# Kernel tuning notes

Hardware: AMD Instinct MI355X
Metric: run time of the kernel (lower is better)

The kernel has to match this reference:

```python
import jax, jax.numpy as jnp
import numpy as np
import math

B, S, K, H, NH = 4, 1024, 512, 1024, 16
HD = H // NH  # 64


def _split_heads(x):
    # [B, L, H] -> [B, NH, L, HD]
    b, l, _ = x.shape
    return x.reshape(b, l, NH, HD).transpose(0, 2, 1, 3)


def setup_inputs() -> dict:
    key = jax.random.key(0)
    ks = jax.random.split(key, 16)
    scale = 1.0 / math.sqrt(H)
    d = {
        'hidden_states': jax.random.normal(ks[0], (B, S, H), jnp.float32),
        'encoder_hidden_states': jax.random.normal(ks[1], (B, K, H), jnp.float32),
        'attention_mask': jnp.zeros((B, 1, 1, S), jnp.float32),
        'encoder_attention_mask': jnp.zeros((B, 1, 1, K), jnp.float32),
    }
    names = ['q', 'k', 'v', 'kq', 'kk', 'kv']
    for i, n in enumerate(names):
        d[f'W{n}'] = jax.random.normal(ks[2 + i], (H, H), jnp.float32) * scale
        d[f'b{n}'] = jnp.zeros((H,), jnp.float32)
    return d


def reference(hidden_states, encoder_hidden_states, attention_mask, encoder_attention_mask,
              Wq, bq, Wk, bk, Wv, bv, Wkq, bkq, Wkk, bkk, Wkv, bkv):
    inv = 1.0 / math.sqrt(HD)
    # self branch
    q = _split_heads(hidden_states @ Wq + bq)            # [B,NH,S,HD]
    k = _split_heads(hidden_states @ Wk + bk)
    v = _split_heads(hidden_states @ Wv + bv)
    scores = jnp.einsum('bhsd,bhtd->bhst', q, k) * inv + attention_mask
    probs = jax.nn.softmax(scores, axis=-1)              # [B,NH,S,S]
    ctx = jnp.einsum('bhst,bhtd->bhsd', probs, v)
    # knowledge branch
    kq = _split_heads(hidden_states @ Wkq + bkq)          # [B,NH,S,HD]
    kk = _split_heads(encoder_hidden_states @ Wkk + bkk)  # [B,NH,K,HD]
    kv = _split_heads(encoder_hidden_states @ Wkv + bkv)
    kscores = jnp.einsum('bhsd,bhtd->bhst', kq, kk) * inv + encoder_attention_mask
    kprobs = jax.nn.softmax(kscores, axis=-1)            # [B,NH,S,K]
    kctx = jnp.einsum('bhst,bhtd->bhsd', kprobs, kv)
    # merge heads and average branches
    out = (ctx + kctx) * 0.5                             # [B,NH,S,HD]
    out = out.transpose(0, 2, 1, 3).reshape(B, S, H)
    return out
```

## Files before the change

### kernel.cpp

```cpp
#include <hip/hip_runtime.h>

#define BATCH 4
#define SEQ   1024
#define KENC  512
#define HDIM  1024
#define NHEAD 16
#define HD    64
#define LOG2E 1.44269504088896340736f

typedef __attribute__((ext_vector_type(8))) short bf16x8;
typedef __attribute__((ext_vector_type(4))) float f32x4;
typedef __attribute__((ext_vector_type(4))) float f4v;
typedef __attribute__((ext_vector_type(4))) short s4v;

__device__ __forceinline__ short f2bf(float f) {
  unsigned u = __float_as_uint(f);
  u += 0x7fffu + ((u >> 16) & 1u);
  return (short)(u >> 16);
}

__device__ __forceinline__ void gload_lds16(const void* g, void* l) {
  __builtin_amdgcn_global_load_lds(
      (const __attribute__((address_space(1))) void*)g,
      (__attribute__((address_space(3))) void*)l, 16, 0, 0);
}

template <int C>
__device__ __forceinline__ float dppf(float x) {
  return __int_as_float(
      __builtin_amdgcn_update_dpp(0, __float_as_int(x), C, 0xF, 0xF, false));
}
__device__ __forceinline__ float red16_max(float x) {
  x = fmaxf(x, dppf<0xB1>(x));
  x = fmaxf(x, dppf<0x4E>(x));
  x = fmaxf(x, dppf<0x141>(x));
  x = fmaxf(x, dppf<0x140>(x));
  return x;
}
__device__ __forceinline__ float red16_sum(float x) {
  x += dppf<0xB1>(x);
  x += dppf<0x4E>(x);
  x += dppf<0x141>(x);
  x += dppf<0x140>(x);
  return x;
}

__global__ __launch_bounds__(256) void cast_bf16(const float* __restrict__ src,
                                                 short* __restrict__ dst, int n4) {
  int i = blockIdx.x * 256 + threadIdx.x;
  if (i >= n4) return;
  f4v v = ((const f4v*)src)[i];
  s4v o;
#pragma unroll
  for (int j = 0; j < 4; ++j) o[j] = f2bf(v[j]);
  ((s4v*)dst)[i] = o;
}

struct WtArgs { const float* W[6]; };

__global__ __launch_bounds__(256) void wt_cast(WtArgs a, short* __restrict__ wt) {
  int j = blockIdx.z;
  const float* W = a.W[j];
  short* dst = wt + (size_t)j * (HDIM * HDIM);
  int cb = blockIdx.x * 32, rb = blockIdx.y * 32;
  __shared__ float t[32][33];
  int tx = threadIdx.x & 31, ty = threadIdx.x >> 5;
#pragma unroll
  for (int rr = 0; rr < 4; ++rr)
    t[ty + rr * 8][tx] = W[(size_t)(rb + ty + rr * 8) * HDIM + cb + tx];
  __syncthreads();
#pragma unroll
  for (int rr = 0; rr < 4; ++rr)
    dst[(size_t)(cb + ty + rr * 8) * HDIM + rb + tx] = f2bf(t[tx][ty + rr * 8]);
}

struct ProjArgs {
  const short* X[6];
  const short* Wt[6];
  const float* bias[6];
  short* out[6];
  int M[6];
  int tshift[6];
  int mode[6];
  float scale[6];
};

__global__ __launch_bounds__(256) void proj_gemm(ProjArgs a) {
  int job = blockIdx.z;
  int M = a.M[job];
  int by = blockIdx.y;
  if (by * 128 >= M) return;
  int bx = blockIdx.x;
  const short* X = a.X[job];
  const short* W = a.Wt[job];

  __shared__ short As[128 * 32];
  __shared__ short Bs[128 * 32];

  int tid = threadIdx.x, lane = tid & 63, wave = tid >> 6;
  int wr = wave >> 1, wc = wave & 1;
  int l15 = lane & 15, g4 = lane >> 4;

  f32x4 acc[4][4];
#pragma unroll
  for (int m = 0; m < 4; ++m)
#pragma unroll
    for (int n = 0; n < 4; ++n)
#pragma unroll
      for (int r = 0; r < 4; ++r) acc[m][n][r] = 0.0f;

  int arow = by * 128, brow = bx * 128;
  const int crow = lane >> 2;
  const int sgrp = (lane & 3) ^ ((lane >> 2) & 3) ^ (lane >> 4);
  const int rsw = (lane & 3) ^ ((l15) >> 2);

  for (int k0 = 0; k0 < HDIM; k0 += 32) {
#pragma unroll
    for (int cc = 0; cc < 2; ++cc) {
      int c = wave * 2 + cc;
      gload_lds16(X + (size_t)(arow + c * 16 + crow) * HDIM + k0 + sgrp * 8,
                  (char*)As + c * 1024);
      gload_lds16(W + (size_t)(brow + c * 16 + crow) * HDIM + k0 + sgrp * 8,
                  (char*)Bs + c * 1024);
    }
    __syncthreads();
    bf16x8 af[4], bfr[4];
#pragma unroll
    for (int m = 0; m < 4; ++m)
      af[m] = *(const bf16x8*)((const char*)As + (wr * 64 + m * 16 + l15) * 64 +
                               ((g4 ^ rsw) << 4));
#pragma unroll
    for (int n = 0; n < 4; ++n)
      bfr[n] = *(const bf16x8*)((const char*)Bs + (wc * 64 + n * 16 + l15) * 64 +
                                ((g4 ^ rsw) << 4));
#pragma unroll
    for (int m = 0; m < 4; ++m)
#pragma unroll
      for (int n = 0; n < 4; ++n)
        acc[m][n] = __builtin_amdgcn_mfma_f32_16x16x32_bf16(af[m], bfr[n],
                                                            acc[m][n], 0, 0, 0);
    __syncthreads();
  }

  const float* bias = a.bias[job];
  short* out = a.out[job];
  int tshift = a.tshift[job], tmask = (1 << tshift) - 1, mode = a.mode[job];
  float scl = a.scale[job];
#pragma unroll
  for (int m = 0; m < 4; ++m) {
    int rowb = arow + wr * 64 + m * 16 + (g4 << 2);
#pragma unroll
    for (int n = 0; n < 4; ++n) {
      int col = brow + wc * 64 + n * 16 + l15;
      float bv = bias[col];
      int head = col >> 6, d = col & 63;
#pragma unroll
      for (int r = 0; r < 4; ++r) {
        int row = rowb + r;
        int bb = row >> tshift, t = row & tmask;
        float val = (acc[m][n][r] + bv) * scl;
        size_t idx;
        if (mode == 0)
          idx = ((((size_t)bb * NHEAD + head) << tshift) + t) * 64 + d;
        else
          idx = ((((size_t)bb * NHEAD + head) * 64 + d) << tshift) + t;
        out[idx] = f2bf(val);
      }
    }
  }
}

__global__ __launch_bounds__(256, 3) void attn_kernel(
    const short* __restrict__ qall, const short* __restrict__ kall,
    const short* __restrict__ vTall, const short* __restrict__ kqall,
    const short* __restrict__ kkall, const short* __restrict__ kvTall,
    const float* __restrict__ amask, const float* __restrict__ emask,
    float* __restrict__ out) {
  __shared__ short Ks[2 * 64 * 64];
  __shared__ short Vs[2 * 64 * 64];
  __shared__ short Ps[4 * 16 * 64];

  int lid = blockIdx.x;
  int id = ((lid & 7) << 7) | (lid >> 3);
  int bh = id >> 4, qb = id & 15;
  int b = bh >> 4, h = bh & 15;
  int lane = threadIdx.x & 63, wave = threadIdx.x >> 6;
  int l15 = lane & 15, g4 = lane >> 4, l7 = lane & 7;
  int srow = lane >> 3;
  int scol = (l7 ^ srow) * 8;
  int qbase = qb * 64;
  char* Pw = (char*)(Ps + wave * 1024);

  const short* qp  = qall  + ((size_t)bh * SEQ + qbase + wave * 16) * 64;
  const short* kqp = kqall + ((size_t)bh * SEQ + qbase + wave * 16) * 64;
  bf16x8 qf0  = *(const bf16x8*)(qp  + l15 * 64 + g4 * 8);
  bf16x8 qf1  = *(const bf16x8*)(qp  + l15 * 64 + 32 + g4 * 8);
  bf16x8 kqf0 = *(const bf16x8*)(kqp + l15 * 64 + g4 * 8);
  bf16x8 kqf1 = *(const bf16x8*)(kqp + l15 * 64 + 32 + g4 * 8);

  const short* kp0 = kall   + (size_t)bh * SEQ * 64;
  const short* vp0 = vTall  + (size_t)bh * 64 * SEQ;
  const short* kp1 = kkall  + (size_t)bh * KENC * 64;
  const short* vp1 = kvTall + (size_t)bh * 64 * KENC;

  bf16x8 qc0 = qf0, qc1 = qf1;
  const float* mpc = amask + (size_t)b * SEQ;

  auto STAGE = [&](int pb, const short* kptr, const short* vptr, int Tt, int kt) {
#pragma unroll
    for (int cc = 0; cc < 2; ++cc) {
      int c = wave * 2 + cc;
      int row = c * 8 + srow;
      gload_lds16(kptr + (size_t)(kt * 64 + row) * 64 + scol,
                  (char*)Ks + pb * 8192 + c * 1024);
      gload_lds16(vptr + (size_t)row * Tt + kt * 64 + scol,
                  (char*)Vs + pb * 8192 + c * 1024);
    }
  };

  STAGE(0, kp0, vp0, SEQ, 0);

  f32x4 ctx[4], c1[4], mr, lr;
#pragma unroll
  for (int i = 0; i < 4; ++i) {
#pragma unroll
    for (int r = 0; r < 4; ++r) { ctx[i][r] = 0.0f; c1[i][r] = 0.0f; }
    mr[i] = -1e30f;
    lr[i] = 0.0f;
  }

#pragma unroll 2
  for (int t = 0; t < 24; ++t) {
    int p = t & 1;
    __syncthreads();
    if (t < 23) {
      int tn = t + 1;
      bool nb = tn >= 16;
      const short* skp = nb ? kp1 : kp0;
      const short* svp = nb ? vp1 : vp0;
      int sT = nb ? KENC : SEQ;
      int skt = nb ? tn - 16 : tn;
      STAGE(p ^ 1, skp, svp, sT, skt);
    }
    if (t == 16) {
#pragma unroll
      for (int dt = 0; dt < 4; ++dt) {
#pragma unroll
        for (int r = 0; r < 4; ++r) {
          c1[dt][r] = ctx[dt][r] * __builtin_amdgcn_rcpf(lr[r]);
          ctx[dt][r] = 0.0f;
        }
      }
#pragma unroll
      for (int r = 0; r < 4; ++r) { mr[r] = -1e30f; lr[r] = 0.0f; }
      qc0 = kqf0;
      qc1 = kqf1;
      mpc = emask + (size_t)b * KENC;
    }
    int kt = (t >= 16) ? t - 16 : t;
    const char* Kb = (const char*)Ks + p * 8192;
    const char* Vb = (const char*)Vs + p * 8192;

    float mk[4];
#pragma unroll
    for (int t2 = 0; t2 < 4; ++t2) mk[t2] = mpc[kt * 64 + t2 * 16 + l15] * LOG2E;

    f32x4 sc[4];
#pragma unroll
    for (int t2 = 0; t2 < 4; ++t2)
#pragma unroll
      for (int r = 0; r < 4; ++r) sc[t2][r] = 0.0f;

    __builtin_amdgcn_s_setprio(1);
#pragma unroll
    for (int t2 = 0; t2 < 4; ++t2) {
      bf16x8 kf0 = *(const bf16x8*)(Kb + (t2 * 16 + l15) * 128 + ((g4 ^ l7) << 4));
      bf16x8 kf1 = *(const bf16x8*)(Kb + (t2 * 16 + l15) * 128 + (((4 + g4) ^ l7) << 4));
      sc[t2] = __builtin_amdgcn_mfma_f32_16x16x32_bf16(qc0, kf0, sc[t2], 0, 0, 0);
      sc[t2] = __builtin_amdgcn_mfma_f32_16x16x32_bf16(qc1, kf1, sc[t2], 0, 0, 0);
    }
    __builtin_amdgcn_s_setprio(0);

#pragma unroll
    for (int t2 = 0; t2 < 4; ++t2)
#pragma unroll
      for (int r = 0; r < 4; ++r) sc[t2][r] += mk[t2];

    f32x4 rm;
#pragma unroll
    for (int r = 0; r < 4; ++r)
      rm[r] = fmaxf(fmaxf(sc[0][r], sc[1][r]), fmaxf(sc[2][r], sc[3][r]));
#pragma unroll
    for (int r = 0; r < 4; ++r) rm[r] = red16_max(rm[r]);

    int need = (rm[0] > mr[0] + 12.f) || (rm[1] > mr[1] + 12.f) ||
               (rm[2] > mr[2] + 12.f) || (rm[3] > mr[3] + 12.f);
    if (__any(need)) {
#pragma unroll
      for (int r = 0; r < 4; ++r) {
        float mn = fmaxf(mr[r], rm[r]);
        float s = __builtin_amdgcn_exp2f(mr[r] - mn);
        mr[r] = mn;
        lr[r] *= s;
        ctx[0][r] *= s; ctx[1][r] *= s; ctx[2][r] *= s; ctx[3][r] *= s;
      }
    }

    f32x4 pv[4], rs;
#pragma unroll
    for (int r = 0; r < 4; ++r) rs[r] = 0.0f;
#pragma unroll
    for (int t2 = 0; t2 < 4; ++t2)
#pragma unroll
      for (int r = 0; r < 4; ++r) {
        pv[t2][r] = __builtin_amdgcn_exp2f(sc[t2][r] - mr[r]);
        rs[r] += pv[t2][r];
      }
#pragma unroll
    for (int r = 0; r < 4; ++r) lr[r] += red16_sum(rs[r]);

#pragma unroll
    for (int t2 = 0; t2 < 4; ++t2) {
      int gg = t2 * 2 + (l15 >> 3);
#pragma unroll
      for (int r4 = 0; r4 < 4; ++r4) {
        int rr = g4 * 4 + r4;
        *(short*)(Pw + rr * 128 + (((gg ^ (rr & 7)) << 4) | (l7 * 2))) =
            f2bf(pv[t2][r4]);
      }
    }
    __builtin_amdgcn_s_setprio(1);
#pragma unroll
    for (int kc = 0; kc < 2; ++kc) {
      bf16x8 pf = *(const bf16x8*)(Pw + l15 * 128 + (((kc * 4 + g4) ^ l7) << 4));
#pragma unroll
      for (int dt = 0; dt < 4; ++dt) {
        bf16x8 vf = *(const bf16x8*)(Vb + (dt * 16 + l15) * 128 +
                                     (((kc * 4 + g4) ^ l7) << 4));
        ctx[dt] = __builtin_amdgcn_mfma_f32_16x16x32_bf16(pf, vf, ctx[dt], 0, 0, 0);
      }
    }
    __builtin_amdgcn_s_setprio(0);
  }

#pragma unroll
  for (int dt = 0; dt < 4; ++dt)
#pragma unroll
    for (int r = 0; r < 4; ++r) {
      float v2 = ctx[dt][r] * __builtin_amdgcn_rcpf(lr[r]);
      int s = qbase + wave * 16 + g4 * 4 + r;
      int d = dt * 16 + l15;
      out[((size_t)b * SEQ + s) * HDIM + h * 64 + d] = 0.5f * (c1[dt][r] + v2);
    }
}

extern "C" void kernel_launch(void* const* d_in, const int* in_sizes, int n_in,
                              void* d_out, int out_size, void* d_ws, size_t ws_size,
                              hipStream_t stream) {
  const float* hid = (const float*)d_in[0];
  const float* enc = (const float*)d_in[1];
  const float* amask = (const float*)d_in[2];
  const float* emask = (const float*)d_in[3];

  char* ws = (char*)d_ws;
  short* hbf = (short*)(ws);
  short* ebf = (short*)(ws + (8u << 20));
  short* wt = (short*)(ws + (12u << 20));
  short* qo = (short*)(ws + (24u << 20));
  short* ko = (short*)(ws + (32u << 20));
  short* vT = (short*)(ws + (40u << 20));
  short* kqo = (short*)(ws + (48u << 20));
  short* kko = (short*)(ws + (56u << 20));
  short* kvT = (short*)(ws + (60u << 20));

  cast_bf16<<<4096, 256, 0, stream>>>(hid, hbf, (BATCH * SEQ * HDIM) / 4);
  cast_bf16<<<2048, 256, 0, stream>>>(enc, ebf, (BATCH * KENC * HDIM) / 4);

  WtArgs wa;
  for (int j = 0; j < 6; ++j) wa.W[j] = (const float*)d_in[4 + 2 * j];
  wt_cast<<<dim3(32, 32, 6), 256, 0, stream>>>(wa, wt);

  ProjArgs pa;
  const short* Xs[6] = {hbf, hbf, hbf, hbf, ebf, ebf};
  short* outs[6] = {qo, ko, vT, kqo, kko, kvT};
  const int Ms[6] = {4096, 4096, 4096, 4096, 2048, 2048};
  const int tsh[6] = {10, 10, 10, 10, 9, 9};
  const int md[6] = {0, 0, 1, 0, 0, 1};
  const float qscale = 0.125f * LOG2E;
  const float scl[6] = {qscale, 1.f, 1.f, qscale, 1.f, 1.f};
  for (int j = 0; j < 6; ++j) {
    pa.X[j] = Xs[j];
    pa.Wt[j] = wt + (size_t)j * (HDIM * HDIM);
    pa.bias[j] = (const float*)d_in[5 + 2 * j];
    pa.out[j] = outs[j];
    pa.M[j] = Ms[j];
    pa.tshift[j] = tsh[j];
    pa.mode[j] = md[j];
    pa.scale[j] = scl[j];
  }
  proj_gemm<<<dim3(8, 32, 6), 256, 0, stream>>>(pa);

  attn_kernel<<<1024, 256, 0, stream>>>(qo, ko, vT, kqo, kko, kvT, amask, emask,
                                        (float*)d_out);
}
```

Baseline: 151.6 us.

## Fuse projection GEMMs into two wide 256x256 tiles with 4-stage LDS pipeline

Replaces the six-job 128x128 projection GEMM with two fused GEMMs: hidden states times four concatenated weights (N=4096) and encoder states times two (N=2048). It uses 256x256 tiles with 8 waves, a 4-deep LDS ring fed by async global-to-LDS loads over 64-element K steps, and split phases that interleave loads with MFMA under priority boosts. The intent is more operand reuse per byte loaded, overlap of loads with compute, and fewer blocks. In exchange it needs 128KB of LDS and many more accumulator registers, which limits occupancy, and 320 blocks may fill the CUs unevenly.

```diff
diff --git a/kernel.cpp b/kernel.cpp
--- a/kernel.cpp
+++ b/kernel.cpp
@@ -74,100 +74,170 @@
     dst[(size_t)(cb + ty + rr * 8) * HDIM + rb + tx] = f2bf(t[tx][ty + rr * 8]);
 }
 
-struct ProjArgs {
-  const short* X[6];
-  const short* Wt[6];
+struct GemmArgs {
+  const short* X[2];
+  const short* W[2];
   const float* bias[6];
   short* out[6];
-  int M[6];
-  int tshift[6];
-  int mode[6];
   float scale[6];
 };
 
-__global__ __launch_bounds__(256) void proj_gemm(ProjArgs a) {
-  int job = blockIdx.z;
-  int M = a.M[job];
-  int by = blockIdx.y;
-  if (by * 128 >= M) return;
-  int bx = blockIdx.x;
-  const short* X = a.X[job];
-  const short* W = a.Wt[job];
-
-  __shared__ short As[128 * 32];
-  __shared__ short Bs[128 * 32];
-
-  int tid = threadIdx.x, lane = tid & 63, wave = tid >> 6;
-  int wr = wave >> 1, wc = wave & 1;
+__global__ __launch_bounds__(512, 2) void proj_gemm8(GemmArgs a) {
+  __shared__ __align__(16) char Lds[131072];
+
+  int lid = blockIdx.x;
+  int id = (lid & 7) * 40 + (lid >> 3);
+  int job, bm, bn;
+  if (id < 256) { job = 0; bm = id >> 4; bn = id & 15; }
+  else          { job = 1; int i2 = id - 256; bm = i2 >> 3; bn = i2 & 7; }
+
+  const char* Xp = (const char*)a.X[job];
+  const char* Wp = (const char*)a.W[job];
+
+  int tid = threadIdx.x;
+  int lane = tid & 63, w = tid >> 6;
   int l15 = lane & 15, g4 = lane >> 4;
-
-  f32x4 acc[4][4];
-#pragma unroll
-  for (int m = 0; m < 4; ++m)
+  int wr = w >> 2, wc = w & 3;
+
+  int srow = w * 16 + (lane >> 2);
+  int sslot = (lane & 3) ^ ((lane >> 3) & 3);
+  size_t sa0 = ((size_t)(bm * 256 + srow)) * 2048 + sslot * 16;
+  size_t sa1 = ((size_t)(bm * 256 + 128 + srow)) * 2048 + sslot * 16;
+  size_t sb0 = ((size_t)(bn * 256 + srow)) * 2048 + sslot * 16;
+  size_t sb1 = ((size_t)(bn * 256 + 128 + srow)) * 2048 + sslot * 16;
+  int ldA0 = w * 1024, ldA1 = 8192 + w * 1024;
+  int ldB0 = 16384 + w * 1024, ldB1 = 24576 + w * 1024;
+
+  int slotR = (l15 >> 1) & 3;
+  int aoff = wr * 8192 + l15 * 64 + ((g4 ^ slotR) << 4);
+  int boff = 16384 + (wc >> 1) * 8192 + ((wc & 1) * 64 + l15) * 64 +
+             ((g4 ^ slotR) << 4);
+
+  f32x4 acc[8][4];
+#pragma unroll
+  for (int m = 0; m < 8; ++m)
 #pragma unroll
     for (int n = 0; n < 4; ++n)
 #pragma unroll
       for (int r = 0; r < 4; ++r) acc[m][n][r] = 0.0f;
 
-  int arow = by * 128, brow = bx * 128;
-  const int crow = lane >> 2;
-  const int sgrp = (lane & 3) ^ ((lane >> 2) & 3) ^ (lane >> 4);
-  const int rsw = (lane & 3) ^ ((l15) >> 2);
-
-  for (int k0 = 0; k0 < HDIM; k0 += 32) {
-#pragma unroll
-    for (int cc = 0; cc < 2; ++cc) {
-      int c = wave * 2 + cc;
-      gload_lds16(X + (size_t)(arow + c * 16 + crow) * HDIM + k0 + sgrp * 8,
-                  (char*)As + c * 1024);
-      gload_lds16(W + (size_t)(brow + c * 16 + crow) * HDIM + k0 + sgrp * 8,
-                  (char*)Bs + c * 1024);
-    }
-    __syncthreads();
-    bf16x8 af[4], bfr[4];
-#pragma unroll
-    for (int m = 0; m < 4; ++m)
-      af[m] = *(const bf16x8*)((const char*)As + (wr * 64 + m * 16 + l15) * 64 +
-                               ((g4 ^ rsw) << 4));
-#pragma unroll
-    for (int n = 0; n < 4; ++n)
-      bfr[n] = *(const bf16x8*)((const char*)Bs + (wc * 64 + n * 16 + l15) * 64 +
-                                ((g4 ^ rsw) << 4));
-#pragma unroll
-    for (int m = 0; m < 4; ++m)
-#pragma unroll
-      for (int n = 0; n < 4; ++n)
-        acc[m][n] = __builtin_amdgcn_mfma_f32_16x16x32_bf16(af[m], bfr[n],
-                                                            acc[m][n], 0, 0, 0);
-    __syncthreads();
+#define STG_A(bufo, kof)                                      \
+  do {                                                        \
+    gload_lds16(Xp + sa0 + (kof), Lds + (bufo) + ldA0);       \
+    gload_lds16(Xp + sa1 + (kof), Lds + (bufo) + ldA1);       \
+  } while (0)
+#define STG_B(bufo, kof)                                      \
+  do {                                                        \
+    gload_lds16(Wp + sb0 + (kof), Lds + (bufo) + ldB0);       \
+    gload_lds16(Wp + sb1 + (kof), Lds + (bufo) + ldB1);       \
+  } while (0)
+
+  STG_A(0, 0);       STG_B(0, 0);
+  STG_A(32768, 64);  STG_B(32768, 64);
+  STG_A(65536, 128); STG_B(65536, 128);
+  asm volatile("s_waitcnt vmcnt(8)" ::: "memory");
+  __builtin_amdgcn_s_barrier();
+  asm volatile("" ::: "memory");
+
+  bf16x8 afr[4], bfr[4];
+
+#define PHASE0(bo, DO_STG, sbo, kof)                                           \
+  do {                                                                         \
+    _Pragma("unroll") for (int m = 0; m < 4; ++m)                              \
+        afr[m] = *(const bf16x8*)(Lds + (bo) + m * 1024 + aoff);               \
+    _Pragma("unroll") for (int n = 0; n < 4; ++n)                              \
+        bfr[n] = *(const bf16x8*)(Lds + (bo) + n * 1024 + boff);               \
+    if (DO_STG) STG_A(sbo, kof);                                               \
+    __builtin_amdgcn_s_barrier();                                              \
+    __builtin_amdgcn_s_setprio(1);                                             \
+    _Pragma("unroll") for (int m = 0; m < 4; ++m)                              \
+        _Pragma("unroll") for (int n = 0; n < 4; ++n)                          \
+            acc[m][n] = __builtin_amdgcn_mfma_f32_16x16x32_bf16(               \
+                afr[m], bfr[n], acc[m][n], 0, 0, 0);                           \
+    __builtin_amdgcn_s_setprio(0);                                             \
+    __builtin_amdgcn_s_barrier();                                              \
+  } while (0)
+
+#define PHASE1(bo, DO_STG, sbo, kof, VMW)                                      \
+  do {                                                                         \
+    _Pragma("unroll") for (int m = 0; m < 4; ++m)                              \
+        afr[m] = *(const bf16x8*)(Lds + (bo) + (m + 4) * 1024 + aoff);         \
+    if (DO_STG) STG_B(sbo, kof);                                               \
+    __builtin_amdgcn_s_barrier();                                              \
+    __builtin_amdgcn_s_setprio(1);                                             \
+    _Pragma("unroll") for (int m = 0; m < 4; ++m)                              \
+        _Pragma("unroll") for (int n = 0; n < 4; ++n)                          \
+            acc[m + 4][n] = __builtin_amdgcn_mfma_f32_16x16x32_bf16(           \
+                afr[m], bfr[n], acc[m + 4][n], 0, 0, 0);                       \
+    __builtin_amdgcn_s_setprio(0);                                             \
+    asm volatile(VMW ::: "memory");                                            \
+    __builtin_amdgcn_s_barrier();                                              \
+    asm volatile("" ::: "memory");                                             \
+  } while (0)
+
+#pragma unroll 1
+  for (int t = 0; t < 29; ++t) {
+    int bo = (t & 3) << 15;
+    int sbo = ((t + 3) & 3) << 15;
+    int kof = (t + 3) * 64;
+    PHASE0(bo, 1, sbo, kof);
+    PHASE1(bo, 1, sbo, kof, "s_waitcnt vmcnt(8)");
   }
-
-  const float* bias = a.bias[job];
-  short* out = a.out[job];
-  int tshift = a.tshift[job], tmask = (1 << tshift) - 1, mode = a.mode[job];
-  float scl = a.scale[job];
-#pragma unroll
-  for (int m = 0; m < 4; ++m) {
-    int rowb = arow + wr * 64 + m * 16 + (g4 << 2);
-#pragma unroll
-    for (int n = 0; n < 4; ++n) {
-      int col = brow + wc * 64 + n * 16 + l15;
-      float bv = bias[col];
-      int head = col >> 6, d = col & 63;
-#pragma unroll
-      for (int r = 0; r < 4; ++r) {
-        int row = rowb + r;
-        int bb = row >> tshift, t = row & tmask;
-        float val = (acc[m][n][r] + bv) * scl;
-        size_t idx;
-        if (mode == 0)
-          idx = ((((size_t)bb * NHEAD + head) << tshift) + t) * 64 + d;
-        else
-          idx = ((((size_t)bb * NHEAD + head) * 64 + d) << tshift) + t;
-        out[idx] = f2bf(val);
-      }
-    }
+  PHASE0((29 & 3) << 15, 0, 0, 0);
+  PHASE1((29 & 3) << 15, 0, 0, 0, "s_waitcnt vmcnt(4)");
+  PHASE0((30 & 3) << 15, 0, 0, 0);
+  PHASE1((30 & 3) << 15, 0, 0, 0, "s_waitcnt vmcnt(0)");
+  PHASE0((31 & 3) << 15, 0, 0, 0);
+  PHASE1((31 & 3) << 15, 0, 0, 0, "s_nop 0");
+
+  int hg = bn * 4 + wc;
+  int jj = (job ? 4 : 0) + (hg >> 4);
+  int head = hg & 15;
+  int tsh = job ? 9 : 10;
+  int tmask = (1 << tsh) - 1;
+  const float* bias = a.bias[jj];
+  float scl = a.scale[jj];
+  short* out = a.out[jj];
+  int mode = (jj == 2 || jj == 5) ? 1 : 0;
+
+  float bv[4];
+#pragma unroll
+  for (int n = 0; n < 4; ++n) bv[n] = bias[head * 64 + n * 16 + l15];
+
+  int rowb = bm * 256 + wr * 128 + g4 * 4;
+  if (mode == 0) {
+#pragma unroll
+    for (int m = 0; m < 8; ++m)
+#pragma unroll
+      for (int n = 0; n < 4; ++n) {
+        int d = n * 16 + l15;
+#pragma unroll
+        for (int r = 0; r < 4; ++r) {
+          int row = rowb + m * 16 + r;
+          int bb = row >> tsh, tt = row & tmask;
+          float val = (acc[m][n][r] + bv[n]) * scl;
+          out[((((size_t)bb * NHEAD + head) << tsh) + tt) * 64 + d] = f2bf(val);
+        }
+      }
+  } else {
+#pragma unroll
+    for (int m = 0; m < 8; ++m)
+#pragma unroll
+      for (int n = 0; n < 4; ++n) {
+        int d = n * 16 + l15;
+#pragma unroll
+        for (int r = 0; r < 4; ++r) {
+          int row = rowb + m * 16 + r;
+          int bb = row >> tsh, tt = row & tmask;
+          float val = (acc[m][n][r] + bv[n]) * scl;
+          out[((((size_t)bb * NHEAD + head) * 64 + d) << tsh) + tt] = f2bf(val);
+        }
+      }
   }
+#undef STG_A
+#undef STG_B
+#undef PHASE0
+#undef PHASE1
 }
 
 __global__ __launch_bounds__(256, 3) void attn_kernel(
@@ -380,25 +450,18 @@
   for (int j = 0; j < 6; ++j) wa.W[j] = (const float*)d_in[4 + 2 * j];
   wt_cast<<<dim3(32, 32, 6), 256, 0, stream>>>(wa, wt);
 
-  ProjArgs pa;
-  const short* Xs[6] = {hbf, hbf, hbf, hbf, ebf, ebf};
+  GemmArgs ga;
+  ga.X[0] = hbf; ga.X[1] = ebf;
+  ga.W[0] = wt;  ga.W[1] = wt + (size_t)4 * HDIM * HDIM;
   short* outs[6] = {qo, ko, vT, kqo, kko, kvT};
-  const int Ms[6] = {4096, 4096, 4096, 4096, 2048, 2048};
-  const int tsh[6] = {10, 10, 10, 10, 9, 9};
-  const int md[6] = {0, 0, 1, 0, 0, 1};
   const float qscale = 0.125f * LOG2E;
   const float scl[6] = {qscale, 1.f, 1.f, qscale, 1.f, 1.f};
   for (int j = 0; j < 6; ++j) {
-    pa.X[j] = Xs[j];
-    pa.Wt[j] = wt + (size_t)j * (HDIM * HDIM);
-    pa.bias[j] = (const float*)d_in[5 + 2 * j];
-    pa.out[j] = outs[j];
-    pa.M[j] = Ms[j];
-    pa.tshift[j] = tsh[j];
-    pa.mode[j] = md[j];
-    pa.scale[j] = scl[j];
+    ga.bias[j] = (const float*)d_in[5 + 2 * j];
+    ga.out[j] = outs[j];
+    ga.scale[j] = scl[j];
   }
-  proj_gemm<<<dim3(8, 32, 6), 256, 0, stream>>>(pa);
+  proj_gemm8<<<320, 512, 0, stream>>>(ga);
 
   attn_kernel<<<1024, 256, 0, stream>>>(qo, ko, vT, kqo, kko, kvT, amask, emask,
                                         (float*)d_out);
```

Result: slower. 172.8 us (+13.9%).

## Rewrite attention with 32x32x16 MFMA, 32 query rows per wave, register-resident P

Applied to the files above, without the earlier changes.

Rewrites the attention kernel so each wave handles 32 query rows with 32x32x16 bf16 MFMAs, computing S^T = K·Q^T so each lane holds a single query column. Probabilities are packed to bf16 and exchanged between half-waves with shuffles rather than round-tripping through LDS, and per-row softmax statistics are broadcast through a small shared buffer. Blocks now cover 128 query rows, halving the grid and the number of K/V tile reloads per query. This trades higher register pressure and extra cross-lane shuffles for fewer LDS accesses and denser matrix instructions.

```diff
diff --git a/kernel.cpp b/kernel.cpp
--- a/kernel.cpp
+++ b/kernel.cpp
@@ -10,6 +10,7 @@
 
 typedef __attribute__((ext_vector_type(8))) short bf16x8;
 typedef __attribute__((ext_vector_type(4))) float f32x4;
+typedef __attribute__((ext_vector_type(16))) float f32x16;
 typedef __attribute__((ext_vector_type(4))) float f4v;
 typedef __attribute__((ext_vector_type(4))) short s4v;
 
@@ -23,26 +24,6 @@
   __builtin_amdgcn_global_load_lds(
       (const __attribute__((address_space(1))) void*)g,
       (__attribute__((address_space(3))) void*)l, 16, 0, 0);
-}
-
-template <int C>
-__device__ __forceinline__ float dppf(float x) {
-  return __int_as_float(
-      __builtin_amdgcn_update_dpp(0, __float_as_int(x), C, 0xF, 0xF, false));
-}
-__device__ __forceinline__ float red16_max(float x) {
-  x = fmaxf(x, dppf<0xB1>(x));
-  x = fmaxf(x, dppf<0x4E>(x));
-  x = fmaxf(x, dppf<0x141>(x));
-  x = fmaxf(x, dppf<0x140>(x));
-  return x;
-}
-__device__ __forceinline__ float red16_sum(float x) {
-  x += dppf<0xB1>(x);
-  x += dppf<0x4E>(x);
-  x += dppf<0x141>(x);
-  x += dppf<0x140>(x);
-  return x;
 }
 
 __global__ __launch_bounds__(256) void cast_bf16(const float* __restrict__ src,
@@ -170,188 +151,201 @@
   }
 }
 
-__global__ __launch_bounds__(256, 3) void attn_kernel(
+__global__ __launch_bounds__(256, 3) void attn32(
     const short* __restrict__ qall, const short* __restrict__ kall,
     const short* __restrict__ vTall, const short* __restrict__ kqall,
     const short* __restrict__ kkall, const short* __restrict__ kvTall,
     const float* __restrict__ amask, const float* __restrict__ emask,
     float* __restrict__ out) {
-  __shared__ short Ks[2 * 64 * 64];
-  __shared__ short Vs[2 * 64 * 64];
-  __shared__ short Ps[4 * 16 * 64];
+  __shared__ char KT[2][8192];
+  __shared__ char VT[2][8192];
+  __shared__ float red[4][32];
 
   int lid = blockIdx.x;
-  int id = ((lid & 7) << 7) | (lid >> 3);
-  int bh = id >> 4, qb = id & 15;
+  int id = (lid & 7) * 64 + (lid >> 3);
+  int bh = id >> 3, qb = id & 7;
   int b = bh >> 4, h = bh & 15;
   int lane = threadIdx.x & 63, wave = threadIdx.x >> 6;
-  int l15 = lane & 15, g4 = lane >> 4, l7 = lane & 7;
-  int srow = lane >> 3;
-  int scol = (l7 ^ srow) * 8;
-  int qbase = qb * 64;
-  char* Pw = (char*)(Ps + wave * 1024);
-
-  const short* qp  = qall  + ((size_t)bh * SEQ + qbase + wave * 16) * 64;
-  const short* kqp = kqall + ((size_t)bh * SEQ + qbase + wave * 16) * 64;
-  bf16x8 qf0  = *(const bf16x8*)(qp  + l15 * 64 + g4 * 8);
-  bf16x8 qf1  = *(const bf16x8*)(qp  + l15 * 64 + 32 + g4 * 8);
-  bf16x8 kqf0 = *(const bf16x8*)(kqp + l15 * 64 + g4 * 8);
-  bf16x8 kqf1 = *(const bf16x8*)(kqp + l15 * 64 + 32 + g4 * 8);
-
-  const short* kp0 = kall   + (size_t)bh * SEQ * 64;
-  const short* vp0 = vTall  + (size_t)bh * 64 * SEQ;
-  const short* kp1 = kkall  + (size_t)bh * KENC * 64;
-  const short* vp1 = kvTall + (size_t)bh * 64 * KENC;
-
-  bf16x8 qc0 = qf0, qc1 = qf1;
+  int l31 = lane & 31, hi = lane >> 5, x7 = l31 & 7;
+  int qrow0 = qb * 128 + wave * 32;
+
+  bf16x8 qcur[4];
+  {
+    const short* qp = qall + ((size_t)bh * SEQ + qrow0 + l31) * 64;
+#pragma unroll
+    for (int i = 0; i < 4; ++i)
+      qcur[i] = *(const bf16x8*)(qp + i * 16 + hi * 8);
+  }
+
+  const char* kb0 = (const char*)(kall + (size_t)bh * SEQ * 64);
+  const char* vb0 = (const char*)(vTall + (size_t)bh * 64 * SEQ);
+  const char* kb1 = (const char*)(kkall + (size_t)bh * KENC * 64);
+  const char* vb1 = (const char*)(kvTall + (size_t)bh * 64 * KENC);
   const float* mpc = amask + (size_t)b * SEQ;
 
-  auto STAGE = [&](int pb, const short* kptr, const short* vptr, int Tt, int kt) {
-#pragma unroll
-    for (int cc = 0; cc < 2; ++cc) {
-      int c = wave * 2 + cc;
-      int row = c * 8 + srow;
-      gload_lds16(kptr + (size_t)(kt * 64 + row) * 64 + scol,
-                  (char*)Ks + pb * 8192 + c * 1024);
-      gload_lds16(vptr + (size_t)row * Tt + kt * 64 + scol,
-                  (char*)Vs + pb * 8192 + c * 1024);
+  auto STAGE = [&](int pb, const char* kb, const char* vb, size_t vrowb, int kt) {
+    int t0 = threadIdx.x;
+#pragma unroll
+    for (int c = 0; c < 2; ++c) {
+      int idx = c * 256 + t0;
+      int row = idx >> 3, phys = idx & 7;
+      int lg = phys ^ (row & 7);
+      gload_lds16(kb + ((size_t)(kt * 64 + row)) * 128 + lg * 16,
+                  KT[pb] + idx * 16);
+      gload_lds16(vb + (size_t)row * vrowb + (size_t)kt * 128 + lg * 16,
+                  VT[pb] + idx * 16);
     }
   };
 
-  STAGE(0, kp0, vp0, SEQ, 0);
-
-  f32x4 ctx[4], c1[4], mr, lr;
-#pragma unroll
-  for (int i = 0; i < 4; ++i) {
-#pragma unroll
-    for (int r = 0; r < 4; ++r) { ctx[i][r] = 0.0f; c1[i][r] = 0.0f; }
-    mr[i] = -1e30f;
-    lr[i] = 0.0f;
-  }
-
-#pragma unroll 2
+  STAGE(0, kb0, vb0, SEQ * 2, 0);
+
+  f32x16 ctx0, ctx1, c10, c11;
+#pragma unroll
+  for (int r = 0; r < 16; ++r) { ctx0[r] = 0.f; ctx1[r] = 0.f; c10[r] = 0.f; c11[r] = 0.f; }
+  float mr = -1e30f, lr = 0.f;
+
+#pragma unroll 1
   for (int t = 0; t < 24; ++t) {
     int p = t & 1;
     __syncthreads();
     if (t < 23) {
       int tn = t + 1;
-      bool nb = tn >= 16;
-      const short* skp = nb ? kp1 : kp0;
-      const short* svp = nb ? vp1 : vp0;
-      int sT = nb ? KENC : SEQ;
-      int skt = nb ? tn - 16 : tn;
-      STAGE(p ^ 1, skp, svp, sT, skt);
+      if (tn >= 16) STAGE(p ^ 1, kb1, vb1, KENC * 2, tn - 16);
+      else          STAGE(p ^ 1, kb0, vb0, SEQ * 2, tn);
     }
     if (t == 16) {
-#pragma unroll
-      for (int dt = 0; dt < 4; ++dt) {
-#pragma unroll
-        for (int r = 0; r < 4; ++r) {
-          c1[dt][r] = ctx[dt][r] * __builtin_amdgcn_rcpf(lr[r]);
-          ctx[dt][r] = 0.0f;
+      if (!hi) red[wave][l31] = lr;
+      asm volatile("s_waitcnt lgkmcnt(0)" ::: "memory");
+#pragma unroll
+      for (int r2 = 0; r2 < 4; ++r2) {
+        f4v lv = *(const f4v*)(&red[wave][r2 * 8 + 4 * hi]);
+#pragma unroll
+        for (int j2 = 0; j2 < 4; ++j2) {
+          float li = __builtin_amdgcn_rcpf(lv[j2]);
+          int r = r2 * 4 + j2;
+          c10[r] = ctx0[r] * li;  ctx0[r] = 0.f;
+          c11[r] = ctx1[r] * li;  ctx1[r] = 0.f;
         }
       }
-#pragma unroll
-      for (int r = 0; r < 4; ++r) { mr[r] = -1e30f; lr[r] = 0.0f; }
-      qc0 = kqf0;
-      qc1 = kqf1;
+      mr = -1e30f; lr = 0.f;
+      const short* kqp = kqall + ((size_t)bh * SEQ + qrow0 + l31) * 64;
+#pragma unroll
+      for (int i = 0; i < 4; ++i)
+        qcur[i] = *(const bf16x8*)(kqp + i * 16 + hi * 8);
       mpc = emask + (size_t)b * KENC;
     }
     int kt = (t >= 16) ? t - 16 : t;
-    const char* Kb = (const char*)Ks + p * 8192;
-    const char* Vb = (const char*)Vs + p * 8192;
-
-    float mk[4];
-#pragma unroll
-    for (int t2 = 0; t2 < 4; ++t2) mk[t2] = mpc[kt * 64 + t2 * 16 + l15] * LOG2E;
-
-    f32x4 sc[4];
-#pragma unroll
-    for (int t2 = 0; t2 < 4; ++t2)
-#pragma unroll
-      for (int r = 0; r < 4; ++r) sc[t2][r] = 0.0f;
-
+    const char* Kp = KT[p];
+    const char* Vp = VT[p];
+
+    f32x16 s0, s1;
+#pragma unroll
+    for (int r = 0; r < 16; ++r) { s0[r] = 0.f; s1[r] = 0.f; }
     __builtin_amdgcn_s_setprio(1);
 #pragma unroll
-    for (int t2 = 0; t2 < 4; ++t2) {
-      bf16x8 kf0 = *(const bf16x8*)(Kb + (t2 * 16 + l15) * 128 + ((g4 ^ l7) << 4));
-      bf16x8 kf1 = *(const bf16x8*)(Kb + (t2 * 16 + l15) * 128 + (((4 + g4) ^ l7) << 4));
-      sc[t2] = __builtin_amdgcn_mfma_f32_16x16x32_bf16(qc0, kf0, sc[t2], 0, 0, 0);
-      sc[t2] = __builtin_amdgcn_mfma_f32_16x16x32_bf16(qc1, kf1, sc[t2], 0, 0, 0);
+    for (int i = 0; i < 4; ++i) {
+      bf16x8 kf = *(const bf16x8*)(Kp + (l31)*128 + (((2 * i + hi) ^ x7) << 4));
+      s0 = __builtin_amdgcn_mfma_f32_32x32x16_bf16(kf, qcur[i], s0, 0, 0, 0);
+    }
+#pragma unroll
+    for (int i = 0; i < 4; ++i) {
+      bf16x8 kf = *(const bf16x8*)(Kp + (32 + l31) * 128 + (((2 * i + hi) ^ x7) << 4));
+      s1 = __builtin_amdgcn_mfma_f32_32x32x16_bf16(kf, qcur[i], s1, 0, 0, 0);
     }
     __builtin_amdgcn_s_setprio(0);
 
-#pragma unroll
-    for (int t2 = 0; t2 < 4; ++t2)
-#pragma unroll
-      for (int r = 0; r < 4; ++r) sc[t2][r] += mk[t2];
-
-    f32x4 rm;
-#pragma unroll
-    for (int r = 0; r < 4; ++r)
-      rm[r] = fmaxf(fmaxf(sc[0][r], sc[1][r]), fmaxf(sc[2][r], sc[3][r]));
-#pragma unroll
-    for (int r = 0; r < 4; ++r) rm[r] = red16_max(rm[r]);
-
-    int need = (rm[0] > mr[0] + 12.f) || (rm[1] > mr[1] + 12.f) ||
-               (rm[2] > mr[2] + 12.f) || (rm[3] > mr[3] + 12.f);
-    if (__any(need)) {
-#pragma unroll
-      for (int r = 0; r < 4; ++r) {
-        float mn = fmaxf(mr[r], rm[r]);
-        float s = __builtin_amdgcn_exp2f(mr[r] - mn);
-        mr[r] = mn;
-        lr[r] *= s;
-        ctx[0][r] *= s; ctx[1][r] *= s; ctx[2][r] *= s; ctx[3][r] *= s;
-      }
-    }
-
-    f32x4 pv[4], rs;
-#pragma unroll
-    for (int r = 0; r < 4; ++r) rs[r] = 0.0f;
-#pragma unroll
-    for (int t2 = 0; t2 < 4; ++t2)
-#pragma unroll
-      for (int r = 0; r < 4; ++r) {
-        pv[t2][r] = __builtin_amdgcn_exp2f(sc[t2][r] - mr[r]);
-        rs[r] += pv[t2][r];
-      }
-#pragma unroll
-    for (int r = 0; r < 4; ++r) lr[r] += red16_sum(rs[r]);
-
-#pragma unroll
-    for (int t2 = 0; t2 < 4; ++t2) {
-      int gg = t2 * 2 + (l15 >> 3);
-#pragma unroll
-      for (int r4 = 0; r4 < 4; ++r4) {
-        int rr = g4 * 4 + r4;
-        *(short*)(Pw + rr * 128 + (((gg ^ (rr & 7)) << 4) | (l7 * 2))) =
-            f2bf(pv[t2][r4]);
-      }
-    }
-    __builtin_amdgcn_s_setprio(1);
-#pragma unroll
-    for (int kc = 0; kc < 2; ++kc) {
-      bf16x8 pf = *(const bf16x8*)(Pw + l15 * 128 + (((kc * 4 + g4) ^ l7) << 4));
-#pragma unroll
-      for (int dt = 0; dt < 4; ++dt) {
-        bf16x8 vf = *(const bf16x8*)(Vb + (dt * 16 + l15) * 128 +
-                                     (((kc * 4 + g4) ^ l7) << 4));
-        ctx[dt] = __builtin_amdgcn_mfma_f32_16x16x32_bf16(pf, vf, ctx[dt], 0, 0, 0);
-      }
-    }
-    __builtin_amdgcn_s_setprio(0);
-  }
-
-#pragma unroll
-  for (int dt = 0; dt < 4; ++dt)
-#pragma unroll
-    for (int r = 0; r < 4; ++r) {
-      float v2 = ctx[dt][r] * __builtin_amdgcn_rcpf(lr[r]);
-      int s = qbase + wave * 16 + g4 * 4 + r;
-      int d = dt * 16 + l15;
-      out[((size_t)b * SEQ + s) * HDIM + h * 64 + d] = 0.5f * (c1[dt][r] + v2);
-    }
+    const float* mp = mpc + kt * 64;
+#pragma unroll
+    for (int r2 = 0; r2 < 4; ++r2) {
+      f4v ma = *(const f4v*)(mp + r2 * 8 + 4 * hi);
+      f4v mb = *(const f4v*)(mp + 32 + r2 * 8 + 4 * hi);
+#pragma unroll
+      for (int j2 = 0; j2 < 4; ++j2) {
+        s0[r2 * 4 + j2] = fmaf(ma[j2], LOG2E, s0[r2 * 4 + j2]);
+        s1[r2 * 4 + j2] = fmaf(mb[j2], LOG2E, s1[r2 * 4 + j2]);
+      }
+    }
+
+    float mx = s0[0];
+#pragma unroll
+    for (int r = 1; r < 16; ++r) mx = fmaxf(mx, s0[r]);
+#pragma unroll
+    for (int r = 0; r < 16; ++r) mx = fmaxf(mx, s1[r]);
+    mx = fmaxf(mx, __int_as_float(__shfl_xor(__float_as_int(mx), 32)));
+
+    if (!__all(mx <= mr + 12.f)) {
+      float mn = fmaxf(mr, mx);
+      float scl = __builtin_amdgcn_exp2f(mr - mn);
+      mr = mn; lr *= scl;
+      if (!hi) red[wave][l31] = scl;
+      asm volatile("s_waitcnt lgkmcnt(0)" ::: "memory");
+#pragma unroll
+      for (int r2 = 0; r2 < 4; ++r2) {
+        f4v sv = *(const f4v*)(&red[wave][r2 * 8 + 4 * hi]);
+#pragma unroll
+        for (int j2 = 0; j2 < 4; ++j2) {
+          ctx0[r2 * 4 + j2] *= sv[j2];
+          ctx1[r2 * 4 + j2] *= sv[j2];
+        }
+      }
+    }
+
+    float rs = 0.f;
+#pragma unroll
+    for (int r = 0; r < 16; ++r) { s0[r] = __builtin_amdgcn_exp2f(s0[r] - mr); rs += s0[r]; }
+#pragma unroll
+    for (int r = 0; r < 16; ++r) { s1[r] = __builtin_amdgcn_exp2f(s1[r] - mr); rs += s1[r]; }
+    rs += __int_as_float(__shfl_xor(__float_as_int(rs), 32));
+    lr += rs;
+
+#pragma unroll
+    for (int s = 0; s < 2; ++s) {
+      const f32x16& sv = s ? s1 : s0;
+      unsigned W[8];
+#pragma unroll
+      for (int r2 = 0; r2 < 4; ++r2) {
+        asm("v_cvt_pk_bf16_f32 %0, %1, %2"
+            : "=v"(W[r2 * 2]) : "v"(sv[r2 * 4 + 0]), "v"(sv[r2 * 4 + 1]));
+        asm("v_cvt_pk_bf16_f32 %0, %1, %2"
+            : "=v"(W[r2 * 2 + 1]) : "v"(sv[r2 * 4 + 2]), "v"(sv[r2 * 4 + 3]));
+      }
+#pragma unroll
+      for (int jr = 0; jr < 2; ++jr) {
+        unsigned sendA = hi ? W[(2 * jr) * 2]     : W[(2 * jr + 1) * 2];
+        unsigned sendB = hi ? W[(2 * jr) * 2 + 1] : W[(2 * jr + 1) * 2 + 1];
+        unsigned rA = (unsigned)__shfl_xor((int)sendA, 32);
+        unsigned rB = (unsigned)__shfl_xor((int)sendB, 32);
+        union { unsigned u[4]; bf16x8 v; } pa;
+        if (!hi) { pa.u[0] = W[2 * jr * 2]; pa.u[1] = W[2 * jr * 2 + 1];
+                   pa.u[2] = rA;            pa.u[3] = rB; }
+        else     { pa.u[0] = rA;            pa.u[1] = rB;
+                   pa.u[2] = W[(2 * jr + 1) * 2]; pa.u[3] = W[(2 * jr + 1) * 2 + 1]; }
+        int j = s * 2 + jr;
+        __builtin_amdgcn_s_setprio(1);
+        bf16x8 vf0 = *(const bf16x8*)(Vp + (l31)*128 + (((2 * j + hi) ^ x7) << 4));
+        ctx0 = __builtin_amdgcn_mfma_f32_32x32x16_bf16(pa.v, vf0, ctx0, 0, 0, 0);
+        bf16x8 vf1 = *(const bf16x8*)(Vp + (32 + l31) * 128 + (((2 * j + hi) ^ x7) << 4));
+        ctx1 = __builtin_amdgcn_mfma_f32_32x32x16_bf16(pa.v, vf1, ctx1, 0, 0, 0);
+        __builtin_amdgcn_s_setprio(0);
+      }
+    }
+  }
+
+  if (!hi) red[wave][l31] = lr;
+  asm volatile("s_waitcnt lgkmcnt(0)" ::: "memory");
+  float* op = out + ((size_t)b * SEQ) * HDIM + h * 64 + l31;
+#pragma unroll
+  for (int r2 = 0; r2 < 4; ++r2) {
+    f4v lv = *(const f4v*)(&red[wave][r2 * 8 + 4 * hi]);
+#pragma unroll
+    for (int j2 = 0; j2 < 4; ++j2) {
+      float li = __builtin_amdgcn_rcpf(lv[j2]);
+      int s = qrow0 + r2 * 8 + 4 * hi + j2;
+      int r = r2 * 4 + j2;
+      op[(size_t)s * HDIM]      = 0.5f * (c10[r] + ctx0[r] * li);
+      op[(size_t)s * HDIM + 32] = 0.5f * (c11[r] + ctx1[r] * li);
+    }
+  }
 }
 
 extern "C" void kernel_launch(void* const* d_in, const int* in_sizes, int n_in,
@@ -400,6 +394,6 @@
   }
   proj_gemm<<<dim3(8, 32, 6), 256, 0, stream>>>(pa);
 
-  attn_kernel<<<1024, 256, 0, stream>>>(qo, ko, vT, kqo, kko, kvT, amask, emask,
-                                        (float*)d_out);
-}
+  attn32<<<512, 256, 0, stream>>>(qo, ko, vT, kqo, kko, kvT, amask, emask,
+                                  (float*)d_out);
+}
```

Result: faster. 147.6 us (-2.6%).
